# Optimization experiments

Hardware: AMD Instinct MI355X
Metric: run time of the kernel (lower is better)

Reference implementation:

```python
import jax, jax.numpy as jnp
import numpy as np

T, B, I, H = 1024, 256, 256, 256
SIGMA = 0.01


def setup_inputs() -> dict:
    key = jax.random.key(0)
    k1, k2, k3 = jax.random.split(key, 3)
    inputs = jax.random.normal(k1, (T, B, I), dtype=jnp.float32)
    W_xh = jax.random.normal(k2, (I, H), dtype=jnp.float32) * SIGMA
    W_hh = jax.random.normal(k3, (H, H), dtype=jnp.float32) * SIGMA
    b_h = jnp.zeros((H,), dtype=jnp.float32)
    return {"inputs": inputs, "W_xh": W_xh, "W_hh": W_hh, "b_h": b_h}


def reference(inputs, W_xh, W_hh, b_h):
    # inputs: [T, B, I]; initial state zeros([B, H]) as in the torch module.
    state0 = jnp.zeros((inputs.shape[1], W_hh.shape[0]), dtype=inputs.dtype)

    def step(state, x_t):
        new_state = jnp.tanh(x_t @ W_xh + state @ W_hh + b_h)
        return new_state, new_state

    state, outputs = jax.lax.scan(step, state0, inputs)
    # outputs: [T, B, H] (stacked per-timestep hidden states), state: [B, H]
    return outputs, state
```

## Files before the change

kernel.cpp:

```cpp
#include <hip/hip_runtime.h>


#define TT 1024
#define BB 256
#define HH 256

typedef __attribute__((ext_vector_type(8))) _Float16 f16x8;
typedef __attribute__((ext_vector_type(4))) _Float16 f16x4;
typedef __attribute__((ext_vector_type(2))) _Float16 f16x2;
typedef __attribute__((ext_vector_type(4))) float f32x4;

__device__ __forceinline__ float fast_tanh(float x) {
    float e = __expf(2.0f * x);
    return 1.0f - 2.0f * __builtin_amdgcn_rcpf(e + 1.0f);
}

template <bool TOWS>
__global__ __launch_bounds__(256, 2) void xw_gemm(const float* __restrict__ X,
                                                  const float* __restrict__ W,
                                                  const float* __restrict__ bh,
                                                  _Float16* __restrict__ ws,
                                                  float* __restrict__ out) {
    const int tid  = threadIdx.x;
    const int lane = tid & 63;
    const int wave = tid >> 6;
    const int c    = lane & 15;
    const int quad = lane >> 4;
    const int hf   = blockIdx.y;
    const int nb   = hf * 128 + wave * 32;

    f16x8 bfx[2][8];
#pragma unroll
    for (int nt = 0; nt < 2; nt++) {
        const int n = nb + nt * 16 + c;
#pragma unroll
        for (int kt = 0; kt < 8; kt++) {
            const int kb = kt * 32 + quad * 8;
            f16x8 v;
#pragma unroll
            for (int j = 0; j < 8; j++)
                v[j] = (_Float16)W[(size_t)(kb + j) * HH + n];
            bfx[nt][kt] = v;
        }
    }
    float bb[2];
#pragma unroll
    for (int nt = 0; nt < 2; nt++) bb[nt] = bh[nb + nt * 16 + c];

    const int ntiles = (TT * BB) / 16;
    for (int rt = blockIdx.x; rt < ntiles; rt += gridDim.x) {
        const float* xp = X + ((size_t)rt * 16 + c) * HH + quad * 8;
        f16x8 af[8];
#pragma unroll
        for (int kt = 0; kt < 8; kt++) {
            float4 lo = *(const float4*)(xp + kt * 32);
            float4 hi = *(const float4*)(xp + kt * 32 + 4);
            f16x8 v;
            v[0] = (_Float16)lo.x; v[1] = (_Float16)lo.y;
            v[2] = (_Float16)lo.z; v[3] = (_Float16)lo.w;
            v[4] = (_Float16)hi.x; v[5] = (_Float16)hi.y;
            v[6] = (_Float16)hi.z; v[7] = (_Float16)hi.w;
            af[kt] = v;
        }

        f32x4 acc[2];
#pragma unroll
        for (int nt = 0; nt < 2; nt++) acc[nt] = (f32x4){0.f, 0.f, 0.f, 0.f};
#pragma unroll
        for (int kt = 0; kt < 8; kt++)
#pragma unroll
            for (int nt = 0; nt < 2; nt++)
                acc[nt] = __builtin_amdgcn_mfma_f32_16x16x32_f16(af[kt], bfx[nt][kt], acc[nt], 0, 0, 0);

        if (TOWS) {
            const int pbase = (hf * 2 + (wave >> 1)) * 64 + c * 4 + (wave & 1) * 2;
#pragma unroll
            for (int i = 0; i < 4; i++) {
                const size_t R = (size_t)rt * 16 + quad * 4 + i;
                f16x2 v;
                v[0] = (_Float16)(acc[0][i] + bb[0]);
                v[1] = (_Float16)(acc[1][i] + bb[1]);
                *(f16x2*)(ws + R * HH + pbase) = v;
            }
        } else {
#pragma unroll
            for (int i = 0; i < 4; i++) {
                const size_t R = (size_t)rt * 16 + quad * 4 + i;
#pragma unroll
                for (int nt = 0; nt < 2; nt++)
                    out[R * HH + nb + nt * 16 + c] = acc[nt][i] + bb[nt];
            }
        }
    }
}

#define SP 272

#define STEP(T, XWH, XWF, CUR, NXT)                                               \
    {                                                                             \
        f16x8 af[8];             \
        _Pragma("unroll")                                                         \
        for (int kt = 0; kt < 8; kt++)                                            \
            af[kt] = *(const f16x8*)&st[CUR][r][kt * 32 + quad * 8];              \
        f32x4 accE[4], accO[4];                                                   \
        _Pragma("unroll")                                                         \
        for (int nt = 0; nt < 4; nt++) {                                          \
            float xv;                                                             \
            if constexpr (FROMWS) xv = (float)XWH[nt]; else xv = XWF[nt];         \
            accE[nt] = (f32x4){xv, 0.f, 0.f, 0.f};                                \
            accO[nt] = (f32x4){0.f, 0.f, 0.f, 0.f};                               \
        }                                                                         \
                 \
        {                                                                         \
            const int tp = ((T) + 2 > TT - 1) ? (TT - 1) : ((T) + 2);             \
            if constexpr (FROMWS) {                                               \
                XWH = *(const f16x4*)(ws + (size_t)tp * (BB * HH) + wsoff);       \
            } else {                                                              \
                _Pragma("unroll")                                                 \
                for (int nt = 0; nt < 4; nt++)                                    \
                    XWF[nt] = out[(size_t)tp * (BB * HH) + colbase + nt * 16];    \
            }                                                                     \
        }                                                                         \
        _Pragma("unroll")                                                         \
        for (int kt = 0; kt < 4; kt++)                                            \
            _Pragma("unroll")                                                     \
            for (int nt = 0; nt < 4; nt++) {                                      \
                accE[nt] = __builtin_amdgcn_mfma_f32_16x16x32_f16(af[2 * kt],     bf[nt][2 * kt],     accE[nt], 0, 0, 0); \
                accO[nt] = __builtin_amdgcn_mfma_f32_16x16x32_f16(af[2 * kt + 1], bf[nt][2 * kt + 1], accO[nt], 0, 0, 0); \
            }                                                                     \
        const size_t obase = (size_t)(T) * (BB * HH) + colbase;                   \
        _Pragma("unroll")                                                         \
        for (int nt = 0; nt < 4; nt++) {                                          \
            h[nt] = fast_tanh(accE[nt][0] + accO[nt][0]);                         \
            out[obase + nt * 16] = h[nt];                                         \
            st[NXT][quad][wave * 64 + nt * 16 + c] = (_Float16)h[nt];             \
        }                                                                         \
        asm volatile("s_waitcnt lgkmcnt(0)" ::: "memory");                        \
        __builtin_amdgcn_s_barrier();                                             \
        __builtin_amdgcn_sched_barrier(0);                                        \
    }

template <bool FROMWS>
__global__ __launch_bounds__(256, 1) void rnn_rec_mfma(const float* __restrict__ Whh,
                                                       const _Float16* __restrict__ ws,
                                                       float* __restrict__ out) {
    __shared__ alignas(16) _Float16 st[2][4][SP];

    const int tid  = threadIdx.x;
    const int lane = tid & 63;
    const int wave = tid >> 6;
    const int c    = lane & 15;
    const int quad = lane >> 4;
    const int b0   = blockIdx.x * 4;

    f16x8 bf[4][8];
#pragma unroll
    for (int nt = 0; nt < 4; nt++) {
        const int n = wave * 64 + nt * 16 + c;
#pragma unroll
        for (int kt = 0; kt < 8; kt++) {
            const int kb = kt * 32 + quad * 8;
            f16x8 v;
#pragma unroll
            for (int j = 0; j < 8; j++)
                v[j] = (_Float16)Whh[(size_t)(kb + j) * HH + n];
            bf[nt][kt] = v;
        }
    }

    for (int i = tid; i < 2 * 4 * SP; i += 256)
        ((_Float16*)st)[i] = (_Float16)0.f;

    const int r = c >> 2;

    const size_t colbase = (size_t)(b0 + quad) * HH + wave * 64 + c;
    const size_t wsoff   = (size_t)(b0 + quad) * HH + wave * 64 + c * 4;

    f16x4 xwhA, xwhB;
    float xwfA[4], xwfB[4];
    if constexpr (FROMWS) {
        xwhA = *(const f16x4*)(ws + wsoff);
        xwhB = *(const f16x4*)(ws + (size_t)BB * HH + wsoff);
    } else {
#pragma unroll
        for (int nt = 0; nt < 4; nt++) xwfA[nt] = out[colbase + nt * 16];
#pragma unroll
        for (int nt = 0; nt < 4; nt++) xwfB[nt] = out[(size_t)BB * HH + colbase + nt * 16];
    }

    asm volatile("s_waitcnt lgkmcnt(0)" ::: "memory");
    __builtin_amdgcn_s_barrier();
    __builtin_amdgcn_sched_barrier(0);

    float h[4] = {0.f, 0.f, 0.f, 0.f};

#pragma unroll 1
    for (int t = 0; t < TT; t += 2) {
        STEP(t,     xwhA, xwfA, 0, 1)
        STEP(t + 1, xwhB, xwfB, 1, 0)
    }

    const size_t fbase = (size_t)TT * (BB * HH) + colbase;
#pragma unroll
    for (int nt = 0; nt < 4; nt++) out[fbase + nt * 16] = h[nt];
}

extern "C" void kernel_launch(void* const* d_in, const int* in_sizes, int n_in,
                              void* d_out, int out_size, void* d_ws, size_t ws_size,
                              hipStream_t stream) {
    const float* X   = (const float*)d_in[0];
    const float* Wxh = (const float*)d_in[1];
    const float* Whh = (const float*)d_in[2];
    const float* bh  = (const float*)d_in[3];
    float* out = (float*)d_out;

    const size_t need = (size_t)TT * BB * HH * sizeof(_Float16);
    if (d_ws != nullptr && ws_size >= need) {
        _Float16* ws = (_Float16*)d_ws;
        xw_gemm<true><<<dim3(2048, 2), dim3(256), 0, stream>>>(X, Wxh, bh, ws, out);
        rnn_rec_mfma<true><<<dim3(BB / 4), dim3(256), 0, stream>>>(Whh, ws, out);
    } else {
        xw_gemm<false><<<dim3(2048, 2), dim3(256), 0, stream>>>(X, Wxh, bh, nullptr, out);
        rnn_rec_mfma<false><<<dim3(BB / 4), dim3(256), 0, stream>>>(Whh, nullptr, out);
    }
}
```

Baseline: 1.132 ms.

## Double-buffer input loads in xw_gemm and pack two batch groups per recurrence block

```diff
diff --git a/kernel.cpp b/kernel.cpp
--- a/kernel.cpp
+++ b/kernel.cpp
@@ -15,8 +15,45 @@
     return 1.0f - 2.0f * __builtin_amdgcn_rcpf(e + 1.0f);
 }
 
+#define AT 16
+
+#define XLOAD(BUF, RT)                                                            \
+    {                                                                             \
+        const float* xp_ = X + ((size_t)(RT)*16 + c) * HH + quad * 8;             \
+        _Pragma("unroll")                                                         \
+        for (int kt = 0; kt < 8; kt++) {                                          \
+            BUF[2 * kt]     = *(const float4*)(xp_ + kt * 32);                    \
+            BUF[2 * kt + 1] = *(const float4*)(xp_ + kt * 32 + 4);                \
+        }                                                                         \
+    }
+
+#define XCOMP(BUF, RT)                                                            \
+    {                                                                             \
+        f16x8 af[8];                                                              \
+        _Pragma("unroll")                                                         \
+        for (int kt = 0; kt < 8; kt++) {                                          \
+            float4 lo = BUF[2 * kt], hi = BUF[2 * kt + 1];                        \
+            f16x8 v;                                                              \
+            v[0] = (_Float16)lo.x; v[1] = (_Float16)lo.y;                         \
+            v[2] = (_Float16)lo.z; v[3] = (_Float16)lo.w;                         \
+            v[4] = (_Float16)hi.x; v[5] = (_Float16)hi.y;                         \
+            v[6] = (_Float16)hi.z; v[7] = (_Float16)hi.w;                         \
+            af[kt] = v;                                                           \
+        }                                                                         \
+        f32x4 acc[2];                                                             \
+        _Pragma("unroll")                                                         \
+        for (int nt = 0; nt < 2; nt++) acc[nt] = (f32x4){0.f, 0.f, 0.f, 0.f};     \
+        _Pragma("unroll")                                                         \
+        for (int kt = 0; kt < 8; kt++)                                            \
+            _Pragma("unroll")                                                     \
+            for (int nt = 0; nt < 2; nt++)                                        \
+                acc[nt] = __builtin_amdgcn_mfma_f32_16x16x32_f16(af[kt], bfx[nt], acc[nt], 0, 0, 0), \
+                bfx[nt] = bfx[nt];                         \
+        (void)0;                                                                  \
+    }
+
 template <bool TOWS>
-__global__ __launch_bounds__(256, 2) void xw_gemm(const float* __restrict__ X,
+__global__ __launch_bounds__(512, 1) void xw_gemm(const float* __restrict__ X,
                                                   const float* __restrict__ W,
                                                   const float* __restrict__ bh,
                                                   _Float16* __restrict__ ws,
@@ -26,8 +63,7 @@
     const int wave = tid >> 6;
     const int c    = lane & 15;
     const int quad = lane >> 4;
-    const int hf   = blockIdx.y;
-    const int nb   = hf * 128 + wave * 32;
+    const int nb   = wave * 32;
 
     f16x8 bfx[2][8];
 #pragma unroll
@@ -47,48 +83,95 @@
 #pragma unroll
     for (int nt = 0; nt < 2; nt++) bb[nt] = bh[nb + nt * 16 + c];
 
-    const int ntiles = (TT * BB) / 16;
-    for (int rt = blockIdx.x; rt < ntiles; rt += gridDim.x) {
-        const float* xp = X + ((size_t)rt * 16 + c) * HH + quad * 8;
-        f16x8 af[8];
-#pragma unroll
-        for (int kt = 0; kt < 8; kt++) {
-            float4 lo = *(const float4*)(xp + kt * 32);
-            float4 hi = *(const float4*)(xp + kt * 32 + 4);
-            f16x8 v;
-            v[0] = (_Float16)lo.x; v[1] = (_Float16)lo.y;
-            v[2] = (_Float16)lo.z; v[3] = (_Float16)lo.w;
-            v[4] = (_Float16)hi.x; v[5] = (_Float16)hi.y;
-            v[6] = (_Float16)hi.z; v[7] = (_Float16)hi.w;
-            af[kt] = v;
+    const int pbase = (wave >> 1) * 64 + c * 4 + (wave & 1) * 2;
+
+    const int base = blockIdx.x * AT;
+
+    float4 bufA[16], bufB[16];
+    XLOAD(bufA, base)
+
+#pragma unroll 1
+    for (int k = 0; k < AT; k += 2) {
+        XLOAD(bufB, base + k + 1)
+        {
+            f16x8 af[8];
+#pragma unroll
+            for (int kt = 0; kt < 8; kt++) {
+                float4 lo = bufA[2 * kt], hi = bufA[2 * kt + 1];
+                f16x8 v;
+                v[0] = (_Float16)lo.x; v[1] = (_Float16)lo.y;
+                v[2] = (_Float16)lo.z; v[3] = (_Float16)lo.w;
+                v[4] = (_Float16)hi.x; v[5] = (_Float16)hi.y;
+                v[6] = (_Float16)hi.z; v[7] = (_Float16)hi.w;
+                af[kt] = v;
+            }
+            f32x4 acc[2];
+#pragma unroll
+            for (int nt = 0; nt < 2; nt++) acc[nt] = (f32x4){0.f, 0.f, 0.f, 0.f};
+#pragma unroll
+            for (int kt = 0; kt < 8; kt++)
+#pragma unroll
+                for (int nt = 0; nt < 2; nt++)
+                    acc[nt] = __builtin_amdgcn_mfma_f32_16x16x32_f16(af[kt], bfx[nt][kt], acc[nt], 0, 0, 0);
+            const int rt = base + k;
+            if (TOWS) {
+#pragma unroll
+                for (int i = 0; i < 4; i++) {
+                    const size_t R = (size_t)rt * 16 + quad * 4 + i;
+                    f16x2 v;
+                    v[0] = (_Float16)(acc[0][i] + bb[0]);
+                    v[1] = (_Float16)(acc[1][i] + bb[1]);
+                    *(f16x2*)(ws + R * HH + pbase) = v;
+                }
+            } else {
+#pragma unroll
+                for (int i = 0; i < 4; i++) {
+                    const size_t R = (size_t)rt * 16 + quad * 4 + i;
+#pragma unroll
+                    for (int nt = 0; nt < 2; nt++)
+                        out[R * HH + nb + nt * 16 + c] = acc[nt][i] + bb[nt];
+                }
+            }
         }
-
-        f32x4 acc[2];
-#pragma unroll
-        for (int nt = 0; nt < 2; nt++) acc[nt] = (f32x4){0.f, 0.f, 0.f, 0.f};
-#pragma unroll
-        for (int kt = 0; kt < 8; kt++)
-#pragma unroll
-            for (int nt = 0; nt < 2; nt++)
-                acc[nt] = __builtin_amdgcn_mfma_f32_16x16x32_f16(af[kt], bfx[nt][kt], acc[nt], 0, 0, 0);
-
-        if (TOWS) {
-            const int pbase = (hf * 2 + (wave >> 1)) * 64 + c * 4 + (wave & 1) * 2;
-#pragma unroll
-            for (int i = 0; i < 4; i++) {
-                const size_t R = (size_t)rt * 16 + quad * 4 + i;
-                f16x2 v;
-                v[0] = (_Float16)(acc[0][i] + bb[0]);
-                v[1] = (_Float16)(acc[1][i] + bb[1]);
-                *(f16x2*)(ws + R * HH + pbase) = v;
+        if (k + 2 < AT) XLOAD(bufA, base + k + 2)
+        {
+            f16x8 af[8];
+#pragma unroll
+            for (int kt = 0; kt < 8; kt++) {
+                float4 lo = bufB[2 * kt], hi = bufB[2 * kt + 1];
+                f16x8 v;
+                v[0] = (_Float16)lo.x; v[1] = (_Float16)lo.y;
+                v[2] = (_Float16)lo.z; v[3] = (_Float16)lo.w;
+                v[4] = (_Float16)hi.x; v[5] = (_Float16)hi.y;
+                v[6] = (_Float16)hi.z; v[7] = (_Float16)hi.w;
+                af[kt] = v;
             }
-        } else {
-#pragma unroll
-            for (int i = 0; i < 4; i++) {
-                const size_t R = (size_t)rt * 16 + quad * 4 + i;
+            f32x4 acc[2];
+#pragma unroll
+            for (int nt = 0; nt < 2; nt++) acc[nt] = (f32x4){0.f, 0.f, 0.f, 0.f};
+#pragma unroll
+            for (int kt = 0; kt < 8; kt++)
 #pragma unroll
                 for (int nt = 0; nt < 2; nt++)
-                    out[R * HH + nb + nt * 16 + c] = acc[nt][i] + bb[nt];
+                    acc[nt] = __builtin_amdgcn_mfma_f32_16x16x32_f16(af[kt], bfx[nt][kt], acc[nt], 0, 0, 0);
+            const int rt = base + k + 1;
+            if (TOWS) {
+#pragma unroll
+                for (int i = 0; i < 4; i++) {
+                    const size_t R = (size_t)rt * 16 + quad * 4 + i;
+                    f16x2 v;
+                    v[0] = (_Float16)(acc[0][i] + bb[0]);
+                    v[1] = (_Float16)(acc[1][i] + bb[1]);
+                    *(f16x2*)(ws + R * HH + pbase) = v;
+                }
+            } else {
+#pragma unroll
+                for (int i = 0; i < 4; i++) {
+                    const size_t R = (size_t)rt * 16 + quad * 4 + i;
+#pragma unroll
+                    for (int nt = 0; nt < 2; nt++)
+                        out[R * HH + nb + nt * 16 + c] = acc[nt][i] + bb[nt];
+                }
             }
         }
     }
@@ -101,7 +184,7 @@
         f16x8 af[8];             \
         _Pragma("unroll")                                                         \
         for (int kt = 0; kt < 8; kt++)                                            \
-            af[kt] = *(const f16x8*)&st[CUR][r][kt * 32 + quad * 8];              \
+            af[kt] = *(const f16x8*)&st[grp][CUR][r][kt * 32 + quad * 8];         \
         f32x4 accE[4], accO[4];                                                   \
         _Pragma("unroll")                                                         \
         for (int nt = 0; nt < 4; nt++) {                                          \
@@ -133,7 +216,7 @@
         for (int nt = 0; nt < 4; nt++) {                                          \
             h[nt] = fast_tanh(accE[nt][0] + accO[nt][0]);                         \
             out[obase + nt * 16] = h[nt];                                         \
-            st[NXT][quad][wave * 64 + nt * 16 + c] = (_Float16)h[nt];             \
+            st[grp][NXT][quad][wg * 64 + nt * 16 + c] = (_Float16)h[nt];          \
         }                                                                         \
         asm volatile("s_waitcnt lgkmcnt(0)" ::: "memory");                        \
         __builtin_amdgcn_s_barrier();                                             \
@@ -141,22 +224,24 @@
     }
 
 template <bool FROMWS>
-__global__ __launch_bounds__(256, 1) void rnn_rec_mfma(const float* __restrict__ Whh,
+__global__ __launch_bounds__(512, 1) void rnn_rec_mfma(const float* __restrict__ Whh,
                                                        const _Float16* __restrict__ ws,
                                                        float* __restrict__ out) {
-    __shared__ alignas(16) _Float16 st[2][4][SP];
+    __shared__ alignas(16) _Float16 st[2][2][4][SP];
 
     const int tid  = threadIdx.x;
     const int lane = tid & 63;
     const int wave = tid >> 6;
+    const int grp  = wave >> 2;
+    const int wg   = wave & 3;
     const int c    = lane & 15;
     const int quad = lane >> 4;
-    const int b0   = blockIdx.x * 4;
+    const int b0   = blockIdx.x * 8 + grp * 4;
 
     f16x8 bf[4][8];
 #pragma unroll
     for (int nt = 0; nt < 4; nt++) {
-        const int n = wave * 64 + nt * 16 + c;
+        const int n = wg * 64 + nt * 16 + c;
 #pragma unroll
         for (int kt = 0; kt < 8; kt++) {
             const int kb = kt * 32 + quad * 8;
@@ -168,13 +253,13 @@
         }
     }
 
-    for (int i = tid; i < 2 * 4 * SP; i += 256)
+    for (int i = tid; i < 2 * 2 * 4 * SP; i += 512)
         ((_Float16*)st)[i] = (_Float16)0.f;
 
     const int r = c >> 2;
 
-    const size_t colbase = (size_t)(b0 + quad) * HH + wave * 64 + c;
-    const size_t wsoff   = (size_t)(b0 + quad) * HH + wave * 64 + c * 4;
+    const size_t colbase = (size_t)(b0 + quad) * HH + wg * 64 + c;
+    const size_t wsoff   = (size_t)(b0 + quad) * HH + wg * 64 + c * 4;
 
     f16x4 xwhA, xwhB;
     float xwfA[4], xwfB[4];
@@ -217,10 +302,10 @@
     const size_t need = (size_t)TT * BB * HH * sizeof(_Float16);
     if (d_ws != nullptr && ws_size >= need) {
         _Float16* ws = (_Float16*)d_ws;
-        xw_gemm<true><<<dim3(2048, 2), dim3(256), 0, stream>>>(X, Wxh, bh, ws, out);
-        rnn_rec_mfma<true><<<dim3(BB / 4), dim3(256), 0, stream>>>(Whh, ws, out);
+        xw_gemm<true><<<dim3((TT * BB / 16) / AT), dim3(512), 0, stream>>>(X, Wxh, bh, ws, out);
+        rnn_rec_mfma<true><<<dim3(BB / 8), dim3(512), 0, stream>>>(Whh, ws, out);
     } else {
-        xw_gemm<false><<<dim3(2048, 2), dim3(256), 0, stream>>>(X, Wxh, bh, nullptr, out);
-        rnn_rec_mfma<false><<<dim3(BB / 4), dim3(256), 0, stream>>>(Whh, nullptr, out);
+        xw_gemm<false><<<dim3((TT * BB / 16) / AT), dim3(512), 0, stream>>>(X, Wxh, bh, nullptr, out);
+        rnn_rec_mfma<false><<<dim3(BB / 8), dim3(512), 0, stream>>>(Whh, nullptr, out);
     }
 }
```

After: 1.336 ms. 18.1% more time.

## Compute all hidden columns per block with LDS double-buffered X staging

Applied to the files above, without the earlier changes.

```diff
diff --git a/kernel.cpp b/kernel.cpp
--- a/kernel.cpp
+++ b/kernel.cpp
@@ -7,13 +7,38 @@
 
 typedef __attribute__((ext_vector_type(8))) _Float16 f16x8;
 typedef __attribute__((ext_vector_type(4))) _Float16 f16x4;
-typedef __attribute__((ext_vector_type(2))) _Float16 f16x2;
 typedef __attribute__((ext_vector_type(4))) float f32x4;
 
 __device__ __forceinline__ float fast_tanh(float x) {
     float e = __expf(2.0f * x);
     return 1.0f - 2.0f * __builtin_amdgcn_rcpf(e + 1.0f);
 }
+
+#define PACK8(DST, LO, HI)                                                        \
+    {                                                                             \
+        f16x8 v_;                                                                 \
+        v_[0] = (_Float16)(LO).x; v_[1] = (_Float16)(LO).y;                       \
+        v_[2] = (_Float16)(LO).z; v_[3] = (_Float16)(LO).w;                       \
+        v_[4] = (_Float16)(HI).x; v_[5] = (_Float16)(HI).y;                       \
+        v_[6] = (_Float16)(HI).z; v_[7] = (_Float16)(HI).w;                       \
+        DST = v_;                                                                 \
+    }
+
+#define AT 8
+
+#define STAGE(BUF, RT)                                                            \
+    {                                                                             \
+        _Pragma("unroll")                                                         \
+        for (int i_ = 0; i_ < 4; i_++) {                                          \
+            const int r_ = wave * 4 + i_;                                         \
+            const float* g_ =                                                     \
+                X + ((size_t)(RT)*16 + r_) * HH + ((lane ^ (r_ & 7)) << 2);       \
+            __builtin_amdgcn_global_load_lds(                                     \
+                (const __attribute__((address_space(1))) void*)g_,                \
+                (__attribute__((address_space(3))) void*)&xs[BUF][r_][0],         \
+                16, 0, 0);                                                        \
+        }                                                                         \
+    }
 
 template <bool TOWS>
 __global__ __launch_bounds__(256, 2) void xw_gemm(const float* __restrict__ X,
@@ -21,18 +46,18 @@
                                                   const float* __restrict__ bh,
                                                   _Float16* __restrict__ ws,
                                                   float* __restrict__ out) {
+    __shared__ float xs[2][16][256];
+
     const int tid  = threadIdx.x;
     const int lane = tid & 63;
     const int wave = tid >> 6;
     const int c    = lane & 15;
     const int quad = lane >> 4;
-    const int hf   = blockIdx.y;
-    const int nb   = hf * 128 + wave * 32;
-
-    f16x8 bfx[2][8];
-#pragma unroll
-    for (int nt = 0; nt < 2; nt++) {
-        const int n = nb + nt * 16 + c;
+
+    f16x8 bfx[4][8];
+#pragma unroll
+    for (int nt = 0; nt < 4; nt++) {
+        const int n = wave * 64 + nt * 16 + c;
 #pragma unroll
         for (int kt = 0; kt < 8; kt++) {
             const int kb = kt * 32 + quad * 8;
@@ -43,54 +68,67 @@
             bfx[nt][kt] = v;
         }
     }
-    float bb[2];
-#pragma unroll
-    for (int nt = 0; nt < 2; nt++) bb[nt] = bh[nb + nt * 16 + c];
-
-    const int ntiles = (TT * BB) / 16;
-    for (int rt = blockIdx.x; rt < ntiles; rt += gridDim.x) {
-        const float* xp = X + ((size_t)rt * 16 + c) * HH + quad * 8;
+    float bb[4];
+#pragma unroll
+    for (int nt = 0; nt < 4; nt++) bb[nt] = bh[wave * 64 + nt * 16 + c];
+
+    const int s  = c & 7;
+    const int t0 = (quad << 1) ^ s;
+    const int t1 = t0 ^ 1;
+
+    const int base = blockIdx.x * AT;
+    int cur = 0;
+
+    STAGE(0, base)
+
+#pragma unroll 1
+    for (int j = 0; j < AT; j++) {
+        const int rt  = base + j;
+        const int nrt = (j + 1 < AT) ? rt + 1 : rt;
+
+        asm volatile("s_barrier" ::: "memory");
+        STAGE(cur ^ 1, nrt)
+        asm volatile("s_waitcnt vmcnt(4)" ::: "memory");
+        asm volatile("s_barrier" ::: "memory");
+        __builtin_amdgcn_sched_barrier(0);
+
+        const float* bp0 = &xs[cur][c][t0 << 2];
+        const float* bp1 = &xs[cur][c][t1 << 2];
         f16x8 af[8];
 #pragma unroll
         for (int kt = 0; kt < 8; kt++) {
-            float4 lo = *(const float4*)(xp + kt * 32);
-            float4 hi = *(const float4*)(xp + kt * 32 + 4);
-            f16x8 v;
-            v[0] = (_Float16)lo.x; v[1] = (_Float16)lo.y;
-            v[2] = (_Float16)lo.z; v[3] = (_Float16)lo.w;
-            v[4] = (_Float16)hi.x; v[5] = (_Float16)hi.y;
-            v[6] = (_Float16)hi.z; v[7] = (_Float16)hi.w;
-            af[kt] = v;
-        }
-
-        f32x4 acc[2];
-#pragma unroll
-        for (int nt = 0; nt < 2; nt++) acc[nt] = (f32x4){0.f, 0.f, 0.f, 0.f};
+            float4 lo = *(const float4*)(bp0 + kt * 32);
+            float4 hi = *(const float4*)(bp1 + kt * 32);
+            PACK8(af[kt], lo, hi)
+        }
+
+        f32x4 acc[4];
+#pragma unroll
+        for (int nt = 0; nt < 4; nt++) acc[nt] = (f32x4){0.f, 0.f, 0.f, 0.f};
 #pragma unroll
         for (int kt = 0; kt < 8; kt++)
 #pragma unroll
-            for (int nt = 0; nt < 2; nt++)
+            for (int nt = 0; nt < 4; nt++)
                 acc[nt] = __builtin_amdgcn_mfma_f32_16x16x32_f16(af[kt], bfx[nt][kt], acc[nt], 0, 0, 0);
 
+        const size_t Rb = (size_t)rt * 16 + quad * 4;
         if (TOWS) {
-            const int pbase = (hf * 2 + (wave >> 1)) * 64 + c * 4 + (wave & 1) * 2;
 #pragma unroll
             for (int i = 0; i < 4; i++) {
-                const size_t R = (size_t)rt * 16 + quad * 4 + i;
-                f16x2 v;
-                v[0] = (_Float16)(acc[0][i] + bb[0]);
-                v[1] = (_Float16)(acc[1][i] + bb[1]);
-                *(f16x2*)(ws + R * HH + pbase) = v;
+                f16x4 v;
+#pragma unroll
+                for (int nt = 0; nt < 4; nt++)
+                    v[nt] = (_Float16)(acc[nt][i] + bb[nt]);
+                *(f16x4*)(ws + (Rb + i) * HH + wave * 64 + c * 4) = v;
             }
         } else {
 #pragma unroll
-            for (int i = 0; i < 4; i++) {
-                const size_t R = (size_t)rt * 16 + quad * 4 + i;
-#pragma unroll
-                for (int nt = 0; nt < 2; nt++)
-                    out[R * HH + nb + nt * 16 + c] = acc[nt][i] + bb[nt];
-            }
-        }
+            for (int i = 0; i < 4; i++)
+#pragma unroll
+                for (int nt = 0; nt < 4; nt++)
+                    out[(Rb + i) * HH + wave * 64 + nt * 16 + c] = acc[nt][i] + bb[nt];
+        }
+        cur ^= 1;
     }
 }
 
@@ -217,10 +255,10 @@
     const size_t need = (size_t)TT * BB * HH * sizeof(_Float16);
     if (d_ws != nullptr && ws_size >= need) {
         _Float16* ws = (_Float16*)d_ws;
-        xw_gemm<true><<<dim3(2048, 2), dim3(256), 0, stream>>>(X, Wxh, bh, ws, out);
+        xw_gemm<true><<<dim3((TT * BB / 16) / AT), dim3(256), 0, stream>>>(X, Wxh, bh, ws, out);
         rnn_rec_mfma<true><<<dim3(BB / 4), dim3(256), 0, stream>>>(Whh, ws, out);
     } else {
-        xw_gemm<false><<<dim3(2048, 2), dim3(256), 0, stream>>>(X, Wxh, bh, nullptr, out);
+        xw_gemm<false><<<dim3((TT * BB / 16) / AT), dim3(256), 0, stream>>>(X, Wxh, bh, nullptr, out);
         rnn_rec_mfma<false><<<dim3(BB / 4), dim3(256), 0, stream>>>(Whh, nullptr, out);
     }
 }
```

After: 984.4 us. 1.15x faster.
